# Kernel tuning notes

Hardware: AMD Instinct MI355X
Metric: run time of the kernel (lower is better)

## Reference

```python
import jax, jax.numpy as jnp
import numpy as np

N = 20000          # num_nodes
R = 48             # num_relations
NB = 12            # num_bases
E = 640000         # num_edges (avg degree 32)
INIT, M1, M2 = 128, 128, 128
OUT3 = 512 - M2 - M1 - INIT  # = 128, per output_size arithmetic in __init__


def setup_inputs() -> dict:
    key = jax.random.key(0)
    ks = jax.random.split(key, 20)
    p = lambda k, shape, s=0.05: jax.random.normal(k, shape, jnp.float32) * s
    return {
        "emb": p(ks[0], (N, INIT)),
        "edge_src": jax.random.randint(ks[1], (E,), 0, N),
        "edge_dst": jax.random.randint(ks[2], (E,), 0, N),
        "edge_types": jax.random.randint(ks[3], (E,), 0, R),
        "comp1": p(ks[4], (R, NB), 0.3), "basis1": p(ks[5], (NB, INIT, M1)),
        "root1": p(ks[6], (INIT, M1)), "bias1": jnp.zeros((M1,), jnp.float32),
        "comp2": p(ks[7], (R, NB), 0.3), "basis2": p(ks[8], (NB, M1, M2)),
        "root2": p(ks[9], (M1, M2)), "bias2": jnp.zeros((M2,), jnp.float32),
        "comp3": p(ks[10], (R, NB), 0.3), "basis3": p(ks[11], (NB, M2, OUT3)),
        "root3": p(ks[12], (M2, OUT3)), "bias3": jnp.zeros((OUT3,), jnp.float32),
    }


def rgcn_conv(x, src, dst, etype, comp, basis, root, bias):
    """PyG RGCNConv with basis decomposition and per-relation mean aggregation.
    out_i = bias + x_i @ root + sum_r W_r^T . mean_{j in N_r(i)} x_j
    Mean aggregation commutes with the linear map, so aggregate raw features per
    (relation, target) first, then apply the relation weights as one batched GEMM.
    """
    Fin = x.shape[1]
    W = jnp.einsum('rb,bio->rio', comp, basis)                 # [R, Fin, Fout]
    seg = etype * N + dst                                      # fused (rel, dst) id
    msg = jax.ops.segment_sum(x[src], seg, num_segments=R * N) # [R*N, Fin]
    cnt = jax.ops.segment_sum(jnp.ones((src.shape[0], 1), x.dtype), seg,
                              num_segments=R * N)
    agg = (msg / jnp.maximum(cnt, 1.0)).reshape(R, N, Fin)     # mean, 0 if no edges
    return jnp.einsum('rni,rio->no', agg, W) + x @ root + bias


def reference(emb, edge_src, edge_dst, edge_types,
              comp1, basis1, root1, bias1,
              comp2, basis2, root2, bias2,
              comp3, basis3, root3, bias3):
    x1 = jax.nn.relu(rgcn_conv(emb, edge_src, edge_dst, edge_types,
                               comp1, basis1, root1, bias1))
    x2 = jax.nn.relu(rgcn_conv(x1, edge_src, edge_dst, edge_types,
                               comp2, basis2, root2, bias2))
    x3 = jax.nn.relu(rgcn_conv(x2, edge_src, edge_dst, edge_types,
                               comp3, basis3, root3, bias3))
    # dropout(0.2) is identity in eval mode
    return jnp.concatenate((x3, x2, x1, emb), axis=1)          # [N, 512]
```

## Files before the change

kernel.cpp:

```cpp
#include <hip/hip_runtime.h>
#include <hip/hip_bf16.h>

#define N_NODES 20000
#define R_REL   48
#define NBASES  12
#define E_EDGES 640000
#define KDIM    1664
#define KSTEPS  52
#define SLOTS   96
#define CPAD    8
#define PF      8

typedef __attribute__((ext_vector_type(8))) short bf16x8;
typedef __attribute__((ext_vector_type(4))) float f32x4;

__device__ inline float loadF(const void* p, long long idx, int isf32) {
    if (isf32 != 0) return ((const float*)p)[idx];
    return __bfloat162float(((const __hip_bfloat16*)p)[idx]);
}

__device__ inline void storeF(void* p, long long idx, int isf32, float v) {
    if (isf32 != 0) ((float*)p)[idx] = v;
    else ((__hip_bfloat16*)p)[idx] = __float2bfloat16(v);
}

__device__ inline unsigned short toBf(float v) {
    __hip_bfloat16 h = __float2bfloat16(v);
    return *(unsigned short*)&h;
}

__global__ void detect_dtype(const void* emb, int* flag) {
    if (threadIdx.x == 0 && blockIdx.x == 0) {
        const unsigned short* h = (const unsigned short*)emb;
        int f32 = 0;
        for (int k = 0; k < 256; k++) {
            unsigned int bits = ((unsigned int)h[k]) << 16;
            float v = __uint_as_float(bits);
            if (!(fabsf(v) < 1000.0f)) f32 = 1;
        }
        *flag = f32;
    }
}

__global__ void zero_i32(int* p, int n) {
    int i = blockIdx.x * 256 + threadIdx.x;
    if (i < n) p[i] = 0;
}

__global__ void scatter_d96(const int* src, const int* dst, const int* typ,
                            int* cursordP, int* s_pack, float* cnt48) {
    int e = blockIdx.x * 256 + threadIdx.x;
    if (e < E_EDGES) {
        int d = dst[e];
        int t = typ[e];
        int pos = atomicAdd(&cursordP[d * CPAD], 1);
        if (pos < SLOTS)
            s_pack[d * SLOTS + pos] = src[e] | (t << 20);
        atomicAdd(&cnt48[d * R_REL + t], 1.0f);
    }
}

__global__ void inv48_kernel(float* p) {
    int i = blockIdx.x * 256 + threadIdx.x;
    float c = p[i];
    p[i] = (c > 0.0f) ? (1.0f / c) : 0.0f;
}

__global__ void build_wcat3(const void* b0, const void* r0,
                            const void* b1, const void* r1,
                            const void* b2, const void* r2,
                            __hip_bfloat16* Wt, const int* flagp) {
    int l = blockIdx.z;
    const void* basis = (l == 0) ? b0 : (l == 1) ? b1 : b2;
    const void* root  = (l == 0) ? r0 : (l == 1) ? r1 : r2;
    int o = blockIdx.x;
    int k = blockIdx.y * 256 + threadIdx.x;
    if (k >= KDIM) return;
    int isf32 = *flagp;
    float v;
    if (k < NBASES * 128) {
        int b = k >> 7, i = k & 127;
        v = loadF(basis, b * 16384 + i * 128 + o, isf32);
    } else {
        v = loadF(root, (k - NBASES * 128) * 128 + o, isf32);
    }
    Wt[(long long)l * (128 * KDIM) + (long long)o * KDIM + k] =
        __float2bfloat16(v);
}

__global__ void copy_emb_xc(const void* emb, void* out, float* xc,
                            const int* flagp) {
    int idx = blockIdx.x * 256 + threadIdx.x;
    int n = idx >> 4;
    int c8 = (idx & 15) * 8;
    float4 f0, f1;
    if (*flagp) {
        const float4* s = (const float4*)((const float*)emb +
                                          (long long)n * 128 + c8);
        f0 = s[0]; f1 = s[1];
        float4* d = (float4*)((float*)out + (long long)n * 512 + 384 + c8);
        d[0] = f0;
        d[1] = f1;
    } else {
        uint4 v = *(const uint4*)((const unsigned short*)emb +
                                  (long long)n * 128 + c8);
        *(uint4*)((unsigned short*)out + (long long)n * 512 + 384 + c8) = v;
        f0.x = __uint_as_float(v.x << 16);
        f0.y = __uint_as_float(v.x & 0xFFFF0000u);
        f0.z = __uint_as_float(v.y << 16);
        f0.w = __uint_as_float(v.y & 0xFFFF0000u);
        f1.x = __uint_as_float(v.z << 16);
        f1.y = __uint_as_float(v.z & 0xFFFF0000u);
        f1.z = __uint_as_float(v.w << 16);
        f1.w = __uint_as_float(v.w & 0xFFFF0000u);
    }
    float4* xd = (float4*)(xc + (long long)n * 128 + c8);
    xd[0] = f0;
    xd[1] = f1;
}

#define FX(j, idx) do {                                                       \
    int p_ = spkw[idx];                                                       \
    pp[j] = p_;                                                               \
    sx[j] = *(const float2*)(xc + (long long)(p_ & 0xFFFFF) * 128 + col);     \
} while (0)

#define CX(j) do {                                                            \
    int rel_ = pp[j] >> 20;                                                   \
    const float* cp_ = &scSw[rel_ * NBASES];                                  \
    float4 cA_ = *(const float4*)cp_;                                         \
    float4 cB_ = *(const float4*)(cp_ + 4);                                   \
    float4 cC_ = *(const float4*)(cp_ + 8);                                   \
    float x0_ = sx[j].x, x1_ = sx[j].y;                                       \
    accA[0]  += cA_.x * x0_;  accB[0]  += cA_.x * x1_;                        \
    accA[1]  += cA_.y * x0_;  accB[1]  += cA_.y * x1_;                        \
    accA[2]  += cA_.z * x0_;  accB[2]  += cA_.z * x1_;                        \
    accA[3]  += cA_.w * x0_;  accB[3]  += cA_.w * x1_;                        \
    accA[4]  += cB_.x * x0_;  accB[4]  += cB_.x * x1_;                        \
    accA[5]  += cB_.y * x0_;  accB[5]  += cB_.y * x1_;                        \
    accA[6]  += cB_.z * x0_;  accB[6]  += cB_.z * x1_;                        \
    accA[7]  += cB_.w * x0_;  accB[7]  += cB_.w * x1_;                        \
    accA[8]  += cC_.x * x0_;  accB[8]  += cC_.x * x1_;                        \
    accA[9]  += cC_.y * x0_;  accB[9]  += cC_.y * x1_;                        \
    accA[10] += cC_.z * x0_;  accB[10] += cC_.z * x1_;                        \
    accA[11] += cC_.w * x0_;  accB[11] += cC_.w * x1_;                        \
} while (0)

__global__ __launch_bounds__(256) void aggregate(
        const int* s_pack, const int* cntP, const float* inv48,
        const void* comp, const float* xc, unsigned short* A,
        const int* flagp) {
    __shared__ float scomp[R_REL * NBASES];
    __shared__ float scS[4][R_REL * NBASES];
    __shared__ int   spk[4][64];
    int isf32 = *flagp;
    int tid = threadIdx.x;
    int lane = tid & 63;
    int w = tid >> 6;
    int dstn = blockIdx.x * 4 + w;

    for (int i = tid; i < R_REL * NBASES; i += 256)
        scomp[i] = loadF(comp, i, isf32);
    __syncthreads();

    int cnt = cntP[dstn * CPAD]; if (cnt > SLOTS) cnt = SLOTS;
    int e0 = dstn * SLOTS;
    int e1 = e0 + cnt;
    int col = lane * 2;
    int* spkw = spk[w];
    float* scSw = scS[w];

    if (lane < R_REL) {
        float iv = inv48[dstn * R_REL + lane];
#pragma unroll
        for (int b = 0; b < NBASES; b++)
            scSw[lane * NBASES + b] = scomp[lane * NBASES + b] * iv;
    }
    asm volatile("s_waitcnt lgkmcnt(0) vmcnt(0)" ::: "memory");

    float accA[NBASES], accB[NBASES];
#pragma unroll
    for (int b = 0; b < NBASES; b++) { accA[b] = 0.0f; accB[b] = 0.0f; }

    for (int c0 = e0; c0 < e1; c0 += 64) {
        {
            int e = c0 + lane;
            spkw[lane] = s_pack[(e < e1) ? e : (e1 - 1)];
        }
        asm volatile("s_waitcnt lgkmcnt(0)" ::: "memory");
        int cn = e1 - c0; if (cn > 64) cn = 64;
        float2 sx[PF]; int pp[PF];
#pragma unroll
        for (int j = 0; j < PF; j++)
            if (j < cn) FX(j, j);
        int i2 = 0;
        for (; i2 + PF <= cn; i2 += PF) {
#pragma unroll
            for (int j = 0; j < PF; j++) {
                CX(j);
                if (i2 + j + PF < cn) FX(j, i2 + j + PF);
            }
        }
#pragma unroll
        for (int j = 0; j < PF; j++)
            if (i2 + j < cn) CX(j);
    }

    unsigned short* Ar = A + (long long)dstn * KDIM;
#pragma unroll
    for (int b = 0; b < NBASES; b++) {
        unsigned int pk = ((unsigned int)toBf(accB[b]) << 16) |
                          (unsigned int)toBf(accA[b]);
        *(unsigned int*)(Ar + b * 128 + col) = pk;
    }
    {
        float2 f = *(const float2*)(xc + (long long)dstn * 128 + col);
        unsigned int pk = ((unsigned int)toBf(f.y) << 16) |
                          (unsigned int)toBf(f.x);
        *(unsigned int*)(Ar + NBASES * 128 + col) = pk;
    }
}

__global__ __launch_bounds__(256) void gemm_out(
        const __hip_bfloat16* A, const __hip_bfloat16* Wt,
        const void* bias, void* out, int slot,
        float* xc, int writeXc, const int* flagp) {
    int isf32 = *flagp;
    int tid = threadIdx.x;
    int lane = tid & 63;
    int w = tid >> 6;
    int lr = lane & 15;
    int lk = lane >> 4;
    int colBase = w * 32;
    int nb = blockIdx.x;
    const __hip_bfloat16* a0p = A + (long long)(nb * 32 + lr) * KDIM;
    const __hip_bfloat16* a1p = a0p + 16 * KDIM;
    const __hip_bfloat16* w0p = Wt + (long long)(colBase + lr) * KDIM;
    const __hip_bfloat16* w1p = w0p + 16 * KDIM;
    f32x4 acc00 = {0.f, 0.f, 0.f, 0.f};
    f32x4 acc01 = {0.f, 0.f, 0.f, 0.f};
    f32x4 acc10 = {0.f, 0.f, 0.f, 0.f};
    f32x4 acc11 = {0.f, 0.f, 0.f, 0.f};
#pragma unroll 4
    for (int ks = 0; ks < KSTEPS; ks++) {
        int ko = ks * 32 + lk * 8;
        bf16x8 a0 = *(const bf16x8*)(a0p + ko);
        bf16x8 a1 = *(const bf16x8*)(a1p + ko);
        bf16x8 b0 = *(const bf16x8*)(w0p + ko);
        bf16x8 b1 = *(const bf16x8*)(w1p + ko);
        acc00 = __builtin_amdgcn_mfma_f32_16x16x32_bf16(a0, b0, acc00, 0, 0, 0);
        acc01 = __builtin_amdgcn_mfma_f32_16x16x32_bf16(a0, b1, acc01, 0, 0, 0);
        acc10 = __builtin_amdgcn_mfma_f32_16x16x32_bf16(a1, b0, acc10, 0, 0, 0);
        acc11 = __builtin_amdgcn_mfma_f32_16x16x32_bf16(a1, b1, acc11, 0, 0, 0);
    }
    float bi0 = loadF(bias, colBase + lr, isf32);
    float bi1 = loadF(bias, colBase + 16 + lr, isf32);
#pragma unroll
    for (int q = 0; q < 4; q++) {
        int row = lk * 4 + q;
        int r0 = nb * 32 + row;
        int r1 = r0 + 16;
        float v00 = fmaxf(acc00[q] + bi0, 0.0f);
        float v01 = fmaxf(acc01[q] + bi1, 0.0f);
        float v10 = fmaxf(acc10[q] + bi0, 0.0f);
        float v11 = fmaxf(acc11[q] + bi1, 0.0f);
        long long n0 = (long long)r0 * 512 + slot;
        long long n1 = (long long)r1 * 512 + slot;
        storeF(out, n0 + colBase + lr,      isf32, v00);
        storeF(out, n0 + colBase + 16 + lr, isf32, v01);
        storeF(out, n1 + colBase + lr,      isf32, v10);
        storeF(out, n1 + colBase + 16 + lr, isf32, v11);
        if (writeXc) {
            xc[(long long)r0 * 128 + colBase + lr]      = v00;
            xc[(long long)r0 * 128 + colBase + 16 + lr] = v01;
            xc[(long long)r1 * 128 + colBase + lr]      = v10;
            xc[(long long)r1 * 128 + colBase + 16 + lr] = v11;
        }
    }
}

extern "C" void kernel_launch(void* const* d_in, const int* in_sizes, int n_in,
                              void* d_out, int out_size, void* d_ws, size_t ws_size,
                              hipStream_t stream) {
    const void* emb  = d_in[0];
    const int* esrc = (const int*)d_in[1];
    const int* edst = (const int*)d_in[2];
    const int* etyp = (const int*)d_in[3];
    const void* comp[3];
    const void* basis[3];
    const void* root[3];
    const void* bias[3];
    for (int l = 0; l < 3; l++) {
        comp[l]  = d_in[4 + l * 4];
        basis[l] = d_in[5 + l * 4];
        root[l]  = d_in[6 + l * 4];
        bias[l]  = d_in[7 + l * 4];
    }

    char* ws = (char*)d_ws;
    int*   flag     = (int*)(ws + 0);
    int*   s_pack   = (int*)(ws + 256);
    int*   cursordP = (int*)(ws + 7680256);
    float* cnt48    = (float*)(ws + 8320256);
    __hip_bfloat16* Wt = (__hip_bfloat16*)(ws + 12160256);
    float* xc       = (float*)(ws + 13438208);
    unsigned short* A = (unsigned short*)(ws + 23678208);

    detect_dtype<<<1, 64, 0, stream>>>(emb, flag);
    zero_i32<<<4375, 256, 0, stream>>>(cursordP, N_NODES * CPAD + N_NODES * R_REL);
    scatter_d96<<<2500, 256, 0, stream>>>(esrc, edst, etyp, cursordP,
                                          s_pack, cnt48);
    inv48_kernel<<<3750, 256, 0, stream>>>(cnt48);
    copy_emb_xc<<<1250, 256, 0, stream>>>(emb, d_out, xc, flag);
    build_wcat3<<<dim3(128, 7, 3), 256, 0, stream>>>(
        basis[0], root[0], basis[1], root[1], basis[2], root[2], Wt, flag);

    const int slots[3] = {256, 128, 0};
    for (int l = 0; l < 3; l++) {
        const __hip_bfloat16* Wtl = Wt + (long long)l * (128 * KDIM);
        aggregate<<<5000, 256, 0, stream>>>(s_pack, cursordP, cnt48, comp[l],
                                            xc, A, flag);
        gemm_out<<<625, 256, 0, stream>>>((const __hip_bfloat16*)A, Wtl,
                                          bias[l], d_out, slots[l],
                                          xc, (l < 2) ? 1 : 0, flag);
    }
    (void)in_sizes; (void)n_in; (void)out_size; (void)ws_size;
}
```

Before: 626.2 us.

## Fuse preprocessing kernels and compute per-relation counts from packed edge lists

Merges dtype detection with zeroing, and the weight build with the embedding copy, into single launches. It removes the global float atomic count per (dst, relation) from the edge scatter and instead recounts relations per destination from the packed slot lists using LDS atomics, writing inverse counts directly. This cuts launch count, drops a zero pass over the count array and avoids contended global atomics. In exchange it adds a pass that rereads the packed lists, and counts are capped at the slot limit.

```diff
diff --git a/kernel.cpp b/kernel.cpp
--- a/kernel.cpp
+++ b/kernel.cpp
@@ -29,8 +29,10 @@
     return *(unsigned short*)&h;
 }
 
-__global__ void detect_dtype(const void* emb, int* flag) {
-    if (threadIdx.x == 0 && blockIdx.x == 0) {
+__global__ void zero_detect(int* p, int n, const void* emb, int* flag) {
+    int i = blockIdx.x * 256 + threadIdx.x;
+    if (i < n) p[i] = 0;
+    if (blockIdx.x == 0 && threadIdx.x == 0) {
         const unsigned short* h = (const unsigned short*)emb;
         int f32 = 0;
         for (int k = 0; k < 256; k++) {
@@ -42,81 +44,96 @@
     }
 }
 
-__global__ void zero_i32(int* p, int n) {
-    int i = blockIdx.x * 256 + threadIdx.x;
-    if (i < n) p[i] = 0;
-}
-
 __global__ void scatter_d96(const int* src, const int* dst, const int* typ,
-                            int* cursordP, int* s_pack, float* cnt48) {
+                            int* cursordP, int* s_pack) {
     int e = blockIdx.x * 256 + threadIdx.x;
     if (e < E_EDGES) {
         int d = dst[e];
-        int t = typ[e];
         int pos = atomicAdd(&cursordP[d * CPAD], 1);
         if (pos < SLOTS)
-            s_pack[d * SLOTS + pos] = src[e] | (t << 20);
-        atomicAdd(&cnt48[d * R_REL + t], 1.0f);
-    }
-}
-
-__global__ void inv48_kernel(float* p) {
-    int i = blockIdx.x * 256 + threadIdx.x;
-    float c = p[i];
-    p[i] = (c > 0.0f) ? (1.0f / c) : 0.0f;
-}
-
-__global__ void build_wcat3(const void* b0, const void* r0,
-                            const void* b1, const void* r1,
-                            const void* b2, const void* r2,
-                            __hip_bfloat16* Wt, const int* flagp) {
-    int l = blockIdx.z;
-    const void* basis = (l == 0) ? b0 : (l == 1) ? b1 : b2;
-    const void* root  = (l == 0) ? r0 : (l == 1) ? r1 : r2;
-    int o = blockIdx.x;
-    int k = blockIdx.y * 256 + threadIdx.x;
-    if (k >= KDIM) return;
+            s_pack[d * SLOTS + pos] = src[e] | (typ[e] << 20);
+    }
+}
+
+__global__ __launch_bounds__(256) void mkinv(const int* s_pack, const int* cntP,
+                                             float* inv48) {
+    __shared__ int shcnt[4][R_REL];
+    int tid = threadIdx.x;
+    int lane = tid & 63;
+    int w = tid >> 6;
+    int d = blockIdx.x * 4 + w;
+    int cnt = cntP[d * CPAD]; if (cnt > SLOTS) cnt = SLOTS;
+    int e0 = d * SLOTS;
+    int e1 = e0 + cnt;
+    if (lane < R_REL) shcnt[w][lane] = 0;
+    asm volatile("s_waitcnt lgkmcnt(0)" ::: "memory");
+    for (int c0 = e0; c0 < e1; c0 += 64) {
+        int e = c0 + lane;
+        if (e < e1) atomicAdd(&shcnt[w][s_pack[e] >> 20], 1);
+    }
+    asm volatile("s_waitcnt lgkmcnt(0) vmcnt(0)" ::: "memory");
+    if (lane < R_REL) {
+        int c = shcnt[w][lane];
+        inv48[(long long)d * R_REL + lane] = (c > 0) ? (1.0f / (float)c) : 0.0f;
+    }
+}
+
+__global__ void copy_build(const void* b0, const void* r0,
+                           const void* b1, const void* r1,
+                           const void* b2, const void* r2,
+                           __hip_bfloat16* Wt,
+                           const void* emb, void* out, float* xc,
+                           const int* flagp) {
+    int z = blockIdx.z;
     int isf32 = *flagp;
-    float v;
-    if (k < NBASES * 128) {
-        int b = k >> 7, i = k & 127;
-        v = loadF(basis, b * 16384 + i * 128 + o, isf32);
+    if (z < 3) {
+        const void* basis = (z == 0) ? b0 : (z == 1) ? b1 : b2;
+        const void* root  = (z == 0) ? r0 : (z == 1) ? r1 : r2;
+        int o = blockIdx.x;
+        int k = blockIdx.y * 256 + threadIdx.x;
+        if (k >= KDIM) return;
+        float v;
+        if (k < NBASES * 128) {
+            int b = k >> 7, i = k & 127;
+            v = loadF(basis, b * 16384 + i * 128 + o, isf32);
+        } else {
+            v = loadF(root, (k - NBASES * 128) * 128 + o, isf32);
+        }
+        Wt[(long long)z * (128 * KDIM) + (long long)o * KDIM + k] =
+            __float2bfloat16(v);
     } else {
-        v = loadF(root, (k - NBASES * 128) * 128 + o, isf32);
-    }
-    Wt[(long long)l * (128 * KDIM) + (long long)o * KDIM + k] =
-        __float2bfloat16(v);
-}
-
-__global__ void copy_emb_xc(const void* emb, void* out, float* xc,
-                            const int* flagp) {
-    int idx = blockIdx.x * 256 + threadIdx.x;
-    int n = idx >> 4;
-    int c8 = (idx & 15) * 8;
-    float4 f0, f1;
-    if (*flagp) {
-        const float4* s = (const float4*)((const float*)emb +
+        int base = (blockIdx.y * 128 + blockIdx.x) * 256 + threadIdx.x;
+        for (int idx = base; idx < N_NODES * 16; idx += 229376) {
+            int n = idx >> 4;
+            int c8 = (idx & 15) * 8;
+            float4 f0, f1;
+            if (isf32) {
+                const float4* s = (const float4*)((const float*)emb +
+                                                  (long long)n * 128 + c8);
+                f0 = s[0]; f1 = s[1];
+                float4* d = (float4*)((float*)out +
+                                      (long long)n * 512 + 384 + c8);
+                d[0] = f0;
+                d[1] = f1;
+            } else {
+                uint4 v = *(const uint4*)((const unsigned short*)emb +
                                           (long long)n * 128 + c8);
-        f0 = s[0]; f1 = s[1];
-        float4* d = (float4*)((float*)out + (long long)n * 512 + 384 + c8);
-        d[0] = f0;
-        d[1] = f1;
-    } else {
-        uint4 v = *(const uint4*)((const unsigned short*)emb +
-                                  (long long)n * 128 + c8);
-        *(uint4*)((unsigned short*)out + (long long)n * 512 + 384 + c8) = v;
-        f0.x = __uint_as_float(v.x << 16);
-        f0.y = __uint_as_float(v.x & 0xFFFF0000u);
-        f0.z = __uint_as_float(v.y << 16);
-        f0.w = __uint_as_float(v.y & 0xFFFF0000u);
-        f1.x = __uint_as_float(v.z << 16);
-        f1.y = __uint_as_float(v.z & 0xFFFF0000u);
-        f1.z = __uint_as_float(v.w << 16);
-        f1.w = __uint_as_float(v.w & 0xFFFF0000u);
-    }
-    float4* xd = (float4*)(xc + (long long)n * 128 + c8);
-    xd[0] = f0;
-    xd[1] = f1;
+                *(uint4*)((unsigned short*)out +
+                          (long long)n * 512 + 384 + c8) = v;
+                f0.x = __uint_as_float(v.x << 16);
+                f0.y = __uint_as_float(v.x & 0xFFFF0000u);
+                f0.z = __uint_as_float(v.y << 16);
+                f0.w = __uint_as_float(v.y & 0xFFFF0000u);
+                f1.x = __uint_as_float(v.z << 16);
+                f1.y = __uint_as_float(v.z & 0xFFFF0000u);
+                f1.z = __uint_as_float(v.w << 16);
+                f1.w = __uint_as_float(v.w & 0xFFFF0000u);
+            }
+            float4* xd = (float4*)(xc + (long long)n * 128 + c8);
+            xd[0] = f0;
+            xd[1] = f1;
+        }
+    }
 }
 
 #define FX(j, idx) do {                                                       \
@@ -301,24 +318,22 @@
     int*   flag     = (int*)(ws + 0);
     int*   s_pack   = (int*)(ws + 256);
     int*   cursordP = (int*)(ws + 7680256);
-    float* cnt48    = (float*)(ws + 8320256);
+    float* inv48    = (float*)(ws + 8320256);
     __hip_bfloat16* Wt = (__hip_bfloat16*)(ws + 12160256);
     float* xc       = (float*)(ws + 13438208);
     unsigned short* A = (unsigned short*)(ws + 23678208);
 
-    detect_dtype<<<1, 64, 0, stream>>>(emb, flag);
-    zero_i32<<<4375, 256, 0, stream>>>(cursordP, N_NODES * CPAD + N_NODES * R_REL);
-    scatter_d96<<<2500, 256, 0, stream>>>(esrc, edst, etyp, cursordP,
-                                          s_pack, cnt48);
-    inv48_kernel<<<3750, 256, 0, stream>>>(cnt48);
-    copy_emb_xc<<<1250, 256, 0, stream>>>(emb, d_out, xc, flag);
-    build_wcat3<<<dim3(128, 7, 3), 256, 0, stream>>>(
-        basis[0], root[0], basis[1], root[1], basis[2], root[2], Wt, flag);
+    zero_detect<<<625, 256, 0, stream>>>(cursordP, N_NODES * CPAD, emb, flag);
+    scatter_d96<<<2500, 256, 0, stream>>>(esrc, edst, etyp, cursordP, s_pack);
+    mkinv<<<5000, 256, 0, stream>>>(s_pack, cursordP, inv48);
+    copy_build<<<dim3(128, 7, 4), 256, 0, stream>>>(
+        basis[0], root[0], basis[1], root[1], basis[2], root[2], Wt,
+        emb, d_out, xc, flag);
 
     const int slots[3] = {256, 128, 0};
     for (int l = 0; l < 3; l++) {
         const __hip_bfloat16* Wtl = Wt + (long long)l * (128 * KDIM);
-        aggregate<<<5000, 256, 0, stream>>>(s_pack, cursordP, cnt48, comp[l],
+        aggregate<<<5000, 256, 0, stream>>>(s_pack, cursordP, inv48, comp[l],
                                             xc, A, flag);
         gemm_out<<<625, 256, 0, stream>>>((const __hip_bfloat16*)A, Wtl,
                                           bias[l], d_out, slots[l],
```

New measurement: 597.6 us. -4.6%, faster.
